# Performance work log

Hardware: AMD Instinct MI355X
Metric: run time of the kernel (lower is better)

## Reference

```python
import jax, jax.numpy as jnp
import numpy as np

N = 100000
E = 1600000
IN_DIM = 128
OUT_DIM = 128
NEG_SLOPE = 0.01  # F.leaky_relu default


def setup_inputs() -> dict:
    key = jax.random.key(0)
    k1, k2, k3, k4, k5, k6 = jax.random.split(key, 6)
    feat = jax.random.normal(k1, (N, IN_DIM), dtype=jnp.float32)
    biclique_mask = jax.random.uniform(k2, (IN_DIM,), dtype=jnp.float32)
    W = jax.random.normal(k3, (OUT_DIM, IN_DIM), dtype=jnp.float32) * 0.05
    attn = jax.random.normal(k4, (OUT_DIM,), dtype=jnp.float32) * 0.1
    src = jax.random.randint(k5, (E,), 0, N, dtype=jnp.int32)
    dst = jax.random.randint(k6, (E,), 0, N, dtype=jnp.int32)
    return {"feat": feat, "biclique_mask": biclique_mask, "W": W,
            "attn": attn, "src": src, "dst": dst}


def reference(feat, biclique_mask, W, attn, src, dst):
    # h = Linear(feat * mask), no bias
    h = (feat * biclique_mask[None, :]) @ W.T            # [N, out_dim]
    # edge score depends only on src node -> compute per-node then gather
    s = jax.nn.leaky_relu(h @ attn, negative_slope=NEG_SLOPE)  # [N]
    score = s[src]                                        # [E]
    # edge softmax grouped by destination node
    seg_max = jax.ops.segment_max(score, dst, num_segments=N)  # [N]
    seg_max = jnp.where(jnp.isfinite(seg_max), seg_max, 0.0)   # empty segs
    ex = jnp.exp(score - seg_max[dst])                     # [E]
    denom = jax.ops.segment_sum(ex, dst, num_segments=N)   # [N]
    a = ex / denom[dst]                                    # [E]
    # weighted aggregation: sum_{e: dst(e)=v} h[src(e)] * a[e]
    m = h[src] * a[:, None]                                # [E, out_dim]
    h_new = jax.ops.segment_sum(m, dst, num_segments=N)    # [N, out_dim]
    return jax.nn.relu(h_new)
```

## Files before the change

### kernel.cpp

```cpp
#include <hip/hip_runtime.h>
#include <math.h>

#define NN 100000
#define EE 1600000
#define DIM 128

#define BK 256
#define NBK2 392
#define NCH 256
#define SCN (NBK2 * NCH)
#define NSB 98

#define N_TILES 782
#define FT_BLOCKS 512
#define HEPB 3125

#define LDS_ROW 272
#define LDS_B_OFF 34816
#define LDS_TOT 69632

#define SRC_MASK 0x1FFFFu

typedef _Float16 half8 __attribute__((ext_vector_type(8)));
typedef _Float16 half4v __attribute__((ext_vector_type(4)));
typedef signed char char8 __attribute__((ext_vector_type(8)));
typedef float f32x4 __attribute__((ext_vector_type(4)));

__global__ __launch_bounds__(256) void k_wt(const float* __restrict__ W,
                                            const float* __restrict__ mask,
                                            _Float16* __restrict__ Bt) {
    int o = blockIdx.x * 256 + threadIdx.x;
    if (o < DIM * DIM) Bt[o] = (_Float16)(W[o] * mask[o & 127]);
}

__global__ __launch_bounds__(512, 4) void k_front(const float* __restrict__ feat,
                                                  const _Float16* __restrict__ Bt,
                                                  const float* __restrict__ attn,
                                                  signed char* __restrict__ hq,
                                                  float* __restrict__ scf,
                                                  _Float16* __restrict__ sv16,
                                                  const int* __restrict__ dst,
                                                  int* __restrict__ gHist) {
    __shared__ char smem[LDS_TOT];
    const int bx = blockIdx.x;
    const int t  = threadIdx.x;
    const int lane = t & 63;
    const int wv   = t >> 6;
    const int l15  = lane & 15;
    const int quad = lane >> 4;

#pragma unroll
    for (int i = 0; i < 4; ++i) {
        int idx = i * FT_BLOCKS + t;
        int r   = idx >> 4;
        int c8  = idx & 15;
        int4 v = ((const int4*)(Bt + (size_t)r * DIM))[c8];
        *(int4*)(smem + LDS_B_OFF + r * LDS_ROW + c8 * 16) = v;
    }

    float avv[8];
#pragma unroll
    for (int nt = 0; nt < 8; ++nt) avv[nt] = attn[nt * 16 + l15];

    for (int tile = bx; tile < N_TILES; tile += FT_BLOCKS) {
        const int rowBase = tile * 128;

#pragma unroll
        for (int i = 0; i < 8; ++i) {
            int idx  = i * FT_BLOCKS + t;
            int r    = idx >> 5;
            int c4   = idx & 31;
            int rowg = rowBase + r;
            float4 f = (rowg < NN)
                           ? ((const float4*)(feat + (size_t)rowg * DIM))[c4]
                           : make_float4(0.f, 0.f, 0.f, 0.f);
            half4v h;
            h[0] = (_Float16)f.x; h[1] = (_Float16)f.y;
            h[2] = (_Float16)f.z; h[3] = (_Float16)f.w;
            *(half4v*)(smem + r * LDS_ROW + c4 * 8) = h;
        }
        __syncthreads();

        const int row0 = rowBase + wv * 16;
        f32x4 acc[8];
#pragma unroll
        for (int nt = 0; nt < 8; ++nt) acc[nt] = (f32x4){0.f, 0.f, 0.f, 0.f};

        const char* Abase = smem + (wv * 16 + l15) * LDS_ROW + quad * 16;
        const char* Bbase = smem + LDS_B_OFF + l15 * LDS_ROW + quad * 16;

#pragma unroll
        for (int kc = 0; kc < 4; ++kc) {
            half8 a = *(const half8*)(Abase + kc * 64);
#pragma unroll
            for (int nt = 0; nt < 8; ++nt) {
                half8 b = *(const half8*)(Bbase + nt * 16 * LDS_ROW + kc * 64);
                acc[nt] = __builtin_amdgcn_mfma_f32_16x16x32_f16(a, b, acc[nt], 0, 0, 0);
            }
        }

        char* qslice = smem + wv * (16 * LDS_ROW);
#pragma unroll
        for (int r = 0; r < 4; ++r) {
            int row = row0 + quad * 4 + r;
            float p = 0.f, m = 0.f;
#pragma unroll
            for (int nt = 0; nt < 8; ++nt) {
                p += acc[nt][r] * avv[nt];
                m = fmaxf(m, fabsf(acc[nt][r]));
            }
            p += __shfl_xor(p, 1, 64);
            p += __shfl_xor(p, 2, 64);
            p += __shfl_xor(p, 4, 64);
            p += __shfl_xor(p, 8, 64);
            m = fmaxf(m, __shfl_xor(m, 1, 64));
            m = fmaxf(m, __shfl_xor(m, 2, 64));
            m = fmaxf(m, __shfl_xor(m, 4, 64));
            m = fmaxf(m, __shfl_xor(m, 8, 64));
            if (l15 == 0 && row < NN) {
                float lr = (p > 0.f) ? p : 0.01f * p;
                sv16[row] = (_Float16)__expf(lr);
                scf[row]  = m * (1.f / 127.f);
            }
            const float inv_s = (m > 0.f) ? (127.f / m) : 0.f;
#pragma unroll
            for (int nt = 0; nt < 8; ++nt) {
                float qv = rintf(acc[nt][r] * inv_s);
                qv = fminf(fmaxf(qv, -127.f), 127.f);
                qslice[(quad * 4 + r) * 128 + nt * 16 + l15] = (signed char)(int)qv;
            }
        }
        {
            const int rowg = row0 + (lane >> 2);
            if (rowg < NN) {
                int4 v0 = *(const int4*)(qslice + lane * 32);
                int4 v1 = *(const int4*)(qslice + lane * 32 + 16);
                int4* dp = (int4*)(hq + (size_t)rowg * DIM + (lane & 3) * 32);
                dp[0] = v0;
                dp[1] = v1;
            }
        }
        __syncthreads();
    }

    int* hist = (int*)smem;
    for (int i = t; i < NBK2; i += FT_BLOCKS) hist[i] = 0;
    __syncthreads();
    const int e0 = bx * HEPB;
    for (int e = e0 + t; e < e0 + HEPB; e += FT_BLOCKS)
        atomicAdd(&hist[dst[e] >> 8], 1);
    __syncthreads();
    const int col = bx >> 1;
    for (int i = t; i < NBK2; i += FT_BLOCKS)
        atomicAdd(&gHist[i * NCH + col], hist[i]);
}

__global__ __launch_bounds__(256) void k_scan_a(const int* __restrict__ deg,
                                                int* __restrict__ excl,
                                                int* __restrict__ bsum) {
    __shared__ int wsum[4];
    __shared__ int woff[4];
    const int t = threadIdx.x, b = blockIdx.x;
    const int base = b * 1024 + t * 4;
    int v0 = deg[base + 0];
    int v1 = deg[base + 1];
    int v2 = deg[base + 2];
    int v3 = deg[base + 3];
    int tsum = v0 + v1 + v2 + v3;

    const int lane = t & 63, w = t >> 6;
    int incl = tsum;
#pragma unroll
    for (int d = 1; d < 64; d <<= 1) {
        int n = __shfl_up(incl, d, 64);
        if (lane >= d) incl += n;
    }
    if (lane == 63) wsum[w] = incl;
    __syncthreads();
    if (t == 0) {
        int run = 0;
#pragma unroll
        for (int i = 0; i < 4; ++i) { woff[i] = run; run += wsum[i]; }
        bsum[b] = run;
    }
    __syncthreads();
    int texcl = incl - tsum + woff[w];
    excl[base + 0] = texcl;
    excl[base + 1] = texcl + v0;
    excl[base + 2] = texcl + v0 + v1;
    excl[base + 3] = texcl + v0 + v1 + v2;
}

#define INLINE_BOFF_SCAN(bsum, sboff, swtop, t)                          \
    {                                                                    \
        const int lane_ = (t) & 63;                                      \
        int v_ = 0, incl_ = 0;                                           \
        if ((t) < 128) {                                                 \
            v_ = ((t) < NSB) ? (bsum)[(t)] : 0;                          \
            incl_ = v_;                                                  \
            _Pragma("unroll")                                            \
            for (int d_ = 1; d_ < 64; d_ <<= 1) {                        \
                int n_ = __shfl_up(incl_, d_, 64);                       \
                if (lane_ >= d_) incl_ += n_;                            \
            }                                                            \
            if ((t) == 63) (swtop) = incl_;                              \
        }                                                                \
        __syncthreads();                                                 \
        if ((t) < NSB) {                                                 \
            int add_ = ((t) >= 64) ? (swtop) : 0;                        \
            (sboff)[(t)] = incl_ - v_ + add_;                            \
        }                                                                \
        __syncthreads();                                                 \
    }

#define EPB 6250
__global__ __launch_bounds__(1024) void k_bscatter(const int* __restrict__ src,
                                                   const int* __restrict__ dst,
                                                   const int* __restrict__ gOff,
                                                   const int* __restrict__ bsum,
                                                   unsigned* __restrict__ binned) {
    __shared__ int cur[NBK2];
    __shared__ int sboff[NSB];
    __shared__ int swtop;
    const int t = threadIdx.x, b = blockIdx.x;

    INLINE_BOFF_SCAN(bsum, sboff, swtop, t)

    for (int i = t; i < NBK2; i += 1024) {
        int idx = i * NCH + b;
        cur[i] = gOff[idx] + sboff[idx >> 10];
    }
    __syncthreads();
    const int e0 = b * EPB;
    int e1 = e0 + EPB; if (e1 > EE) e1 = EE;
    for (int e = e0 + t; e < e1; e += 1024) {
        int d  = dst[e];
        int si = src[e];
        int bk   = d >> 8;
        int dloc = d & (BK - 1);
        int pos = atomicAdd(&cur[bk], 1);
        binned[pos] = (unsigned)si | ((unsigned)dloc << 17);
    }
}

__global__ __launch_bounds__(1024) void k_group(const int* __restrict__ gOff,
                                                const int* __restrict__ bsum,
                                                const unsigned* __restrict__ binned,
                                                const _Float16* __restrict__ sv16,
                                                const float* __restrict__ scf,
                                                unsigned* __restrict__ pack,
                                                int* __restrict__ offs,
                                                float* __restrict__ lsum) {
    __shared__ int ldeg[BK];
    __shared__ float lsumSh[BK];
    __shared__ int wpart[4];
    __shared__ int sboff[NSB];
    __shared__ int swtop;
    const int bk = blockIdx.x;
    const int t  = threadIdx.x;

    INLINE_BOFF_SCAN(bsum, sboff, swtop, t)

    const int i0 = bk * NCH;
    const int base = gOff[i0] + sboff[i0 >> 10];
    int endp;
    if (bk == NBK2 - 1) endp = EE;
    else {
        int i1 = (bk + 1) * NCH;
        endp = gOff[i1] + sboff[i1 >> 10];
    }

    if (t < BK) { ldeg[t] = 0; lsumSh[t] = 0.f; }
    __syncthreads();
    for (int j = base + t; j < endp; j += 1024)
        atomicAdd(&ldeg[(binned[j] >> 17) & (BK - 1)], 1);
    __syncthreads();

    int v = 0, incl = 0;
    const int lane = t & 63;
    if (t < BK) {
        v = ldeg[t];
        incl = v;
#pragma unroll
        for (int d = 1; d < 64; d <<= 1) {
            int n = __shfl_up(incl, d, 64);
            if (lane >= d) incl += n;
        }
        if (lane == 63) wpart[t >> 6] = incl;
    }
    __syncthreads();
    if (t == 0) {
        int run = 0;
#pragma unroll
        for (int i = 0; i < 4; ++i) { int tmp = wpart[i]; wpart[i] = run; run += tmp; }
    }
    __syncthreads();
    if (t < BK) {
        int excl = incl - v + wpart[t >> 6];
        int c = base + excl;
        int n = bk * BK + t;
        if (n < NN) offs[n] = c;
        ldeg[t] = c;
    }
    if (bk == NBK2 - 1 && t == 0) offs[NN] = EE;
    __syncthreads();

    for (int j = base + t; j < endp; j += 1024) {
        unsigned e = binned[j];
        int dloc = (e >> 17) & (BK - 1);
        int si   = e & SRC_MASK;
        float w  = (float)sv16[si];
        float sc = scf[si];
        unsigned short wb =
            __builtin_bit_cast(unsigned short, (_Float16)(w * sc));
        atomicAdd(&lsumSh[dloc], w);
        int pos = atomicAdd(&ldeg[dloc], 1);
        pack[pos] = (unsigned)si | ((unsigned)wb << 17);
    }
    __syncthreads();
    if (t < BK) {
        int n = bk * BK + t;
        if (n < NN) lsum[n] = lsumSh[t];
    }
}

#define TAIL_STEP(S)                                                        \
    {                                                                       \
        int idx_ = p + (S) * 4 + g;                                         \
        bool ok_ = idx_ < end;                                              \
        unsigned eb_ = pack[ok_ ? idx_ : last];                             \
        char8 q_ = *(const char8*)(hb + ((size_t)(eb_ & SRC_MASK) << 7));   \
        float wg_ = ok_ ? (float)__builtin_bit_cast(                        \
                              _Float16, (unsigned short)(eb_ >> 17))        \
                        : 0.f;                                              \
        _Pragma("unroll")                                                   \
        for (int k_ = 0; k_ < 8; ++k_)                                      \
            acc[k_] = fmaf((float)q_[k_], wg_, acc[k_]);                    \
    }

__global__ __launch_bounds__(256) void k_agg(const signed char* __restrict__ hq,
                                             const int* __restrict__ offs,
                                             const unsigned* __restrict__ pack,
                                             const float* __restrict__ lsum,
                                             float* __restrict__ out) {
    const int lane = threadIdx.x & 63;
    const int g    = lane >> 4;
    const int li   = lane & 15;
    const int wid  = __builtin_amdgcn_readfirstlane(blockIdx.x * 4 + (threadIdx.x >> 6));
    if (wid >= NN) return;
    const int beg = __builtin_amdgcn_readfirstlane(offs[wid]);
    const int end = __builtin_amdgcn_readfirstlane(offs[wid + 1]);

    const signed char* hb = hq + li * 8;
    float acc[8];
#pragma unroll
    for (int k = 0; k < 8; ++k) acc[k] = 0.f;

    int p = beg;
    for (; p + 16 <= end; p += 16) {
        unsigned eb[4];
#pragma unroll
        for (int s = 0; s < 4; ++s) eb[s] = pack[p + s * 4 + g];
        char8 q[4];
#pragma unroll
        for (int s = 0; s < 4; ++s)
            q[s] = *(const char8*)(hb + ((size_t)(eb[s] & SRC_MASK) << 7));
        float wg[4];
#pragma unroll
        for (int s = 0; s < 4; ++s)
            wg[s] = (float)__builtin_bit_cast(_Float16,
                                              (unsigned short)(eb[s] >> 17));
#pragma unroll
        for (int s = 0; s < 4; ++s)
#pragma unroll
            for (int k = 0; k < 8; ++k)
                acc[k] = fmaf((float)q[s][k], wg[s], acc[k]);
    }
    const int rem = end - p;
    if (rem > 0) {
        const int last = end - 1;
        if (rem > 12)      { TAIL_STEP(0) TAIL_STEP(1) TAIL_STEP(2) TAIL_STEP(3) }
        else if (rem > 8)  { TAIL_STEP(0) TAIL_STEP(1) TAIL_STEP(2) }
        else if (rem > 4)  { TAIL_STEP(0) TAIL_STEP(1) }
        else               { TAIL_STEP(0) }
    }

#pragma unroll
    for (int k = 0; k < 8; ++k) {
        acc[k] += __shfl_xor(acc[k], 16, 64);
        acc[k] += __shfl_xor(acc[k], 32, 64);
    }

    const float l   = lsum[wid];
    const float inv = (l > 0.f) ? (1.0f / l) : 0.f;

    if (g == 0) {
        float4 o0, o1;
        o0.x = fmaxf(acc[0] * inv, 0.f);
        o0.y = fmaxf(acc[1] * inv, 0.f);
        o0.z = fmaxf(acc[2] * inv, 0.f);
        o0.w = fmaxf(acc[3] * inv, 0.f);
        o1.x = fmaxf(acc[4] * inv, 0.f);
        o1.y = fmaxf(acc[5] * inv, 0.f);
        o1.z = fmaxf(acc[6] * inv, 0.f);
        o1.w = fmaxf(acc[7] * inv, 0.f);
        float4* op = (float4*)(out + (size_t)wid * DIM + li * 8);
        op[0] = o0;
        op[1] = o1;
    }
}

extern "C" void kernel_launch(void* const* d_in, const int* in_sizes, int n_in,
                              void* d_out, int out_size, void* d_ws, size_t ws_size,
                              hipStream_t stream) {
    const float* feat = (const float*)d_in[0];
    const float* mask = (const float*)d_in[1];
    const float* W    = (const float*)d_in[2];
    const float* attn = (const float*)d_in[3];
    const int*   src  = (const int*)d_in[4];
    const int*   dst  = (const int*)d_in[5];
    float* out = (float*)d_out;

    char* ws = (char*)d_ws;
    size_t off = 0;
    auto alloc = [&](size_t bytes) -> void* {
        void* p = ws + off;
        off = (off + bytes + 511) & ~(size_t)511;
        return p;
    };
    signed char* hq  = (signed char*)alloc((size_t)NN * DIM);
    float*   scf  = (float*)alloc((size_t)NN * 4);
    float*   lsum = (float*)alloc((size_t)NN * 4);
    _Float16* sv16 = (_Float16*)alloc((size_t)NN * 2);
    _Float16* Bt   = (_Float16*)alloc((size_t)DIM * DIM * 2);
    int*     gOff  = (int*)alloc((size_t)SCN * 4);
    int*     offs  = (int*)alloc((size_t)(NN + 1) * 4);
    int*     bsum  = (int*)alloc((size_t)NSB * 4);
    unsigned* binned = (unsigned*)alloc((size_t)EE * 4);
    unsigned* pack   = (unsigned*)alloc((size_t)EE * 4);

    hipMemsetAsync(gOff, 0, (size_t)SCN * 4, stream);
    k_wt<<<(DIM * DIM + 255) / 256, 256, 0, stream>>>(W, mask, Bt);
    k_front<<<FT_BLOCKS, 512, 0, stream>>>(feat, Bt, attn, hq, scf,
                                           sv16, dst, gOff);
    k_scan_a<<<NSB, 256, 0, stream>>>(gOff, gOff, bsum);
    k_bscatter<<<NCH, 1024, 0, stream>>>(src, dst, gOff, bsum, binned);
    k_group<<<NBK2, 1024, 0, stream>>>(gOff, bsum, binned, sv16, scf,
                                       pack, offs, lsum);
    k_agg<<<(NN + 3) / 4, 256, 0, stream>>>(hq, offs, pack, lsum, out);
}
```

Measured before the change: 211.6 us.

## Split front kernel into dedicated GEMM and histogram blocks, drop memset

The fused front kernel now launches one block per 128-row GEMM tile plus 256 separate histogram blocks, instead of 512 persistent blocks that looped over tiles and then each did a histogram slice. Histogram blocks own a whole column and write their counts directly, so the global atomics and the memset of the offset array go away. This removes the tail imbalance where some blocks handled two tiles, and lets the histogram work overlap the GEMM. In exchange, each GEMM block reloads the B matrix into LDS.

```diff
diff --git a/kernel.cpp b/kernel.cpp
--- a/kernel.cpp
+++ b/kernel.cpp
@@ -8,12 +8,12 @@
 #define BK 256
 #define NBK2 392
 #define NCH 256
+#define EPB 6250
 #define SCN (NBK2 * NCH)
 #define NSB 98
 
-#define N_TILES 782
-#define FT_BLOCKS 512
-#define HEPB 3125
+#define GEMM_BLKS 782
+#define FBLK 512
 
 #define LDS_ROW 272
 #define LDS_B_OFF 34816
@@ -44,115 +44,116 @@
     __shared__ char smem[LDS_TOT];
     const int bx = blockIdx.x;
     const int t  = threadIdx.x;
+
+    if (bx >= GEMM_BLKS) {
+        int* hist = (int*)smem;
+        const int b = bx - GEMM_BLKS;
+        for (int i = t; i < NBK2; i += FBLK) hist[i] = 0;
+        __syncthreads();
+        const int e0 = b * EPB;
+        int e1 = e0 + EPB; if (e1 > EE) e1 = EE;
+        for (int e = e0 + t; e < e1; e += FBLK)
+            atomicAdd(&hist[dst[e] >> 8], 1);
+        __syncthreads();
+        for (int i = t; i < NBK2; i += FBLK)
+            gHist[i * NCH + b] = hist[i];
+        return;
+    }
+
+    const int rowBase = bx * 128;
+
+#pragma unroll
+    for (int i = 0; i < 8; ++i) {
+        int idx  = i * FBLK + t;
+        int r    = idx >> 5;
+        int c4   = idx & 31;
+        int rowg = rowBase + r;
+        float4 f = (rowg < NN)
+                       ? ((const float4*)(feat + (size_t)rowg * DIM))[c4]
+                       : make_float4(0.f, 0.f, 0.f, 0.f);
+        half4v h;
+        h[0] = (_Float16)f.x; h[1] = (_Float16)f.y;
+        h[2] = (_Float16)f.z; h[3] = (_Float16)f.w;
+        *(half4v*)(smem + r * LDS_ROW + c4 * 8) = h;
+    }
+#pragma unroll
+    for (int i = 0; i < 4; ++i) {
+        int idx = i * FBLK + t;
+        int r   = idx >> 4;
+        int c8  = idx & 15;
+        int4 v = ((const int4*)(Bt + (size_t)r * DIM))[c8];
+        *(int4*)(smem + LDS_B_OFF + r * LDS_ROW + c8 * 16) = v;
+    }
+    __syncthreads();
+
     const int lane = t & 63;
     const int wv   = t >> 6;
     const int l15  = lane & 15;
     const int quad = lane >> 4;
-
-#pragma unroll
-    for (int i = 0; i < 4; ++i) {
-        int idx = i * FT_BLOCKS + t;
-        int r   = idx >> 4;
-        int c8  = idx & 15;
-        int4 v = ((const int4*)(Bt + (size_t)r * DIM))[c8];
-        *(int4*)(smem + LDS_B_OFF + r * LDS_ROW + c8 * 16) = v;
+    const int row0 = rowBase + wv * 16;
+
+    f32x4 acc[8];
+#pragma unroll
+    for (int nt = 0; nt < 8; ++nt) acc[nt] = (f32x4){0.f, 0.f, 0.f, 0.f};
+
+    const char* Abase = smem + (wv * 16 + l15) * LDS_ROW + quad * 16;
+    const char* Bbase = smem + LDS_B_OFF + l15 * LDS_ROW + quad * 16;
+
+#pragma unroll
+    for (int kc = 0; kc < 4; ++kc) {
+        half8 a = *(const half8*)(Abase + kc * 64);
+#pragma unroll
+        for (int nt = 0; nt < 8; ++nt) {
+            half8 b = *(const half8*)(Bbase + nt * 16 * LDS_ROW + kc * 64);
+            acc[nt] = __builtin_amdgcn_mfma_f32_16x16x32_f16(a, b, acc[nt], 0, 0, 0);
+        }
     }
 
     float avv[8];
 #pragma unroll
     for (int nt = 0; nt < 8; ++nt) avv[nt] = attn[nt * 16 + l15];
 
-    for (int tile = bx; tile < N_TILES; tile += FT_BLOCKS) {
-        const int rowBase = tile * 128;
-
-#pragma unroll
-        for (int i = 0; i < 8; ++i) {
-            int idx  = i * FT_BLOCKS + t;
-            int r    = idx >> 5;
-            int c4   = idx & 31;
-            int rowg = rowBase + r;
-            float4 f = (rowg < NN)
-                           ? ((const float4*)(feat + (size_t)rowg * DIM))[c4]
-                           : make_float4(0.f, 0.f, 0.f, 0.f);
-            half4v h;
-            h[0] = (_Float16)f.x; h[1] = (_Float16)f.y;
-            h[2] = (_Float16)f.z; h[3] = (_Float16)f.w;
-            *(half4v*)(smem + r * LDS_ROW + c4 * 8) = h;
-        }
-        __syncthreads();
-
-        const int row0 = rowBase + wv * 16;
-        f32x4 acc[8];
-#pragma unroll
-        for (int nt = 0; nt < 8; ++nt) acc[nt] = (f32x4){0.f, 0.f, 0.f, 0.f};
-
-        const char* Abase = smem + (wv * 16 + l15) * LDS_ROW + quad * 16;
-        const char* Bbase = smem + LDS_B_OFF + l15 * LDS_ROW + quad * 16;
-
-#pragma unroll
-        for (int kc = 0; kc < 4; ++kc) {
-            half8 a = *(const half8*)(Abase + kc * 64);
-#pragma unroll
-            for (int nt = 0; nt < 8; ++nt) {
-                half8 b = *(const half8*)(Bbase + nt * 16 * LDS_ROW + kc * 64);
-                acc[nt] = __builtin_amdgcn_mfma_f32_16x16x32_f16(a, b, acc[nt], 0, 0, 0);
-            }
-        }
-
-        char* qslice = smem + wv * (16 * LDS_ROW);
-#pragma unroll
-        for (int r = 0; r < 4; ++r) {
-            int row = row0 + quad * 4 + r;
-            float p = 0.f, m = 0.f;
-#pragma unroll
-            for (int nt = 0; nt < 8; ++nt) {
-                p += acc[nt][r] * avv[nt];
-                m = fmaxf(m, fabsf(acc[nt][r]));
-            }
-            p += __shfl_xor(p, 1, 64);
-            p += __shfl_xor(p, 2, 64);
-            p += __shfl_xor(p, 4, 64);
-            p += __shfl_xor(p, 8, 64);
-            m = fmaxf(m, __shfl_xor(m, 1, 64));
-            m = fmaxf(m, __shfl_xor(m, 2, 64));
-            m = fmaxf(m, __shfl_xor(m, 4, 64));
-            m = fmaxf(m, __shfl_xor(m, 8, 64));
-            if (l15 == 0 && row < NN) {
-                float lr = (p > 0.f) ? p : 0.01f * p;
-                sv16[row] = (_Float16)__expf(lr);
-                scf[row]  = m * (1.f / 127.f);
-            }
-            const float inv_s = (m > 0.f) ? (127.f / m) : 0.f;
-#pragma unroll
-            for (int nt = 0; nt < 8; ++nt) {
-                float qv = rintf(acc[nt][r] * inv_s);
-                qv = fminf(fmaxf(qv, -127.f), 127.f);
-                qslice[(quad * 4 + r) * 128 + nt * 16 + l15] = (signed char)(int)qv;
-            }
-        }
-        {
-            const int rowg = row0 + (lane >> 2);
-            if (rowg < NN) {
-                int4 v0 = *(const int4*)(qslice + lane * 32);
-                int4 v1 = *(const int4*)(qslice + lane * 32 + 16);
-                int4* dp = (int4*)(hq + (size_t)rowg * DIM + (lane & 3) * 32);
-                dp[0] = v0;
-                dp[1] = v1;
-            }
-        }
-        __syncthreads();
-    }
-
-    int* hist = (int*)smem;
-    for (int i = t; i < NBK2; i += FT_BLOCKS) hist[i] = 0;
-    __syncthreads();
-    const int e0 = bx * HEPB;
-    for (int e = e0 + t; e < e0 + HEPB; e += FT_BLOCKS)
-        atomicAdd(&hist[dst[e] >> 8], 1);
-    __syncthreads();
-    const int col = bx >> 1;
-    for (int i = t; i < NBK2; i += FT_BLOCKS)
-        atomicAdd(&gHist[i * NCH + col], hist[i]);
+    char* qslice = smem + wv * (16 * LDS_ROW);
+#pragma unroll
+    for (int r = 0; r < 4; ++r) {
+        int row = row0 + quad * 4 + r;
+        float p = 0.f, m = 0.f;
+#pragma unroll
+        for (int nt = 0; nt < 8; ++nt) {
+            p += acc[nt][r] * avv[nt];
+            m = fmaxf(m, fabsf(acc[nt][r]));
+        }
+        p += __shfl_xor(p, 1, 64);
+        p += __shfl_xor(p, 2, 64);
+        p += __shfl_xor(p, 4, 64);
+        p += __shfl_xor(p, 8, 64);
+        m = fmaxf(m, __shfl_xor(m, 1, 64));
+        m = fmaxf(m, __shfl_xor(m, 2, 64));
+        m = fmaxf(m, __shfl_xor(m, 4, 64));
+        m = fmaxf(m, __shfl_xor(m, 8, 64));
+        if (l15 == 0 && row < NN) {
+            float lr = (p > 0.f) ? p : 0.01f * p;
+            sv16[row] = (_Float16)__expf(lr);
+            scf[row]  = m * (1.f / 127.f);
+        }
+        const float inv_s = (m > 0.f) ? (127.f / m) : 0.f;
+#pragma unroll
+        for (int nt = 0; nt < 8; ++nt) {
+            float qv = rintf(acc[nt][r] * inv_s);
+            qv = fminf(fmaxf(qv, -127.f), 127.f);
+            qslice[(quad * 4 + r) * 128 + nt * 16 + l15] = (signed char)(int)qv;
+        }
+    }
+    {
+        const int rowg = row0 + (lane >> 2);
+        if (rowg < NN) {
+            int4 v0 = *(const int4*)(qslice + lane * 32);
+            int4 v1 = *(const int4*)(qslice + lane * 32 + 16);
+            int4* dp = (int4*)(hq + (size_t)rowg * DIM + (lane & 3) * 32);
+            dp[0] = v0;
+            dp[1] = v1;
+        }
+    }
 }
 
 __global__ __launch_bounds__(256) void k_scan_a(const int* __restrict__ deg,
@@ -213,7 +214,6 @@
         __syncthreads();                                                 \
     }
 
-#define EPB 6250
 __global__ __launch_bounds__(1024) void k_bscatter(const int* __restrict__ src,
                                                    const int* __restrict__ dst,
                                                    const int* __restrict__ gOff,
@@ -439,10 +439,9 @@
     unsigned* binned = (unsigned*)alloc((size_t)EE * 4);
     unsigned* pack   = (unsigned*)alloc((size_t)EE * 4);
 
-    hipMemsetAsync(gOff, 0, (size_t)SCN * 4, stream);
     k_wt<<<(DIM * DIM + 255) / 256, 256, 0, stream>>>(W, mask, Bt);
-    k_front<<<FT_BLOCKS, 512, 0, stream>>>(feat, Bt, attn, hq, scf,
-                                           sv16, dst, gOff);
+    k_front<<<GEMM_BLKS + NCH, FBLK, 0, stream>>>(feat, Bt, attn, hq, scf,
+                                                  sv16, dst, gOff);
     k_scan_a<<<NSB, 256, 0, stream>>>(gOff, gOff, bsum);
     k_bscatter<<<NCH, 1024, 0, stream>>>(src, dst, gOff, bsum, binned);
     k_group<<<NBK2, 1024, 0, stream>>>(gOff, bsum, binned, sv16, scf,
```

Measured after the change: 203.9 us. -3.6%, faster.
